# Kernel tuning notes

Hardware: AMD Instinct MI355X
Metric: run time of the kernel (lower is better)

The kernel has to match this reference:

```python
import jax, jax.numpy as jnp
import numpy as np

M = 8192        # number of variables (len(z), R is MxM)
MAX_K = 256     # max active components (self.max_k)
THRESH = 0.01   # gamma threshold used to drop topk entries


def setup_inputs() -> dict:
    key = jax.random.key(0)
    ks = jax.random.split(key, 6)
    # R is an LD-correlation-like PSD matrix (required for logdet / inverse)
    A = jax.random.normal(ks[0], (M, M), dtype=jnp.float32)
    R = A @ A.T / M + 0.1 * jnp.eye(M, dtype=jnp.float32)
    z = jax.random.normal(ks[1], (M,), dtype=jnp.float32)
    sigma2 = jax.random.uniform(ks[2], (M,), jnp.float32, 0.05, 1.0)
    p = jax.random.uniform(ks[3], (M,), jnp.float32, 0.01, 0.99)
    pq = jax.random.uniform(ks[4], (M,), jnp.float32, 0.01, 0.99)
    gamma = jax.random.uniform(ks[5], (M,), jnp.float32, 1e-4, 1.0)
    # S = inv(R) @ z, computed once in the module __init__ (a constant buffer)
    S = jnp.linalg.inv(R) @ z
    N = 100000  # GWAS sample size (python int scalar)
    return {"R": R, "z": z, "sigma2": sigma2, "p": p, "pq": pq,
            "gamma": gamma, "S": S, "N": N}


def reference(R, z, sigma2, p, pq, gamma, S, N):
    # topk + threshold filter, expressed with a fixed-size mask (jit-friendly).
    u, ind = jax.lax.top_k(gamma, MAX_K)                  # [MAX_K]
    mask = (u > THRESH).astype(R.dtype)                   # 1 for kept indices
    # U = N * diag(sigma2*gamma)[:, ind] is column-sparse: column j has single
    # nonzero vals[j] at row ind[j]. Masked columns are exactly zero, which
    # makes sigma identity in those columns, so logdet/inverse reduce to the
    # active kxk block -- identical math to the dynamic-k torch version.
    vals = N * sigma2[ind] * gamma[ind] * mask            # [MAX_K]
    Rk = R[ind]                                           # V = R[ind, :], [MAX_K, M]
    Rkk = Rk[:, ind]                                      # [MAX_K, MAX_K]
    # sigma = I_k + V @ U  (V@U collapses to Rkk scaled per-column by vals)
    sigma = jnp.eye(MAX_K, dtype=R.dtype) + Rkk * vals[None, :]
    inv = jnp.linalg.inv(sigma)
    logdet = jnp.linalg.slogdet(sigma)[1]                 # sigma is PD
    # quadratic_form = -z^T (I - U inv V) S / 2, without materializing MxM
    zU = z[ind] * vals                                    # z^T U, [MAX_K]
    VS = Rk @ S                                           # V S,   [MAX_K]
    quadratic_form = -(z @ S - zU @ (inv @ VS)) / 2
    log_likelihood = -logdet / 2 + quadratic_form
    # Bernoulli KL over the active set
    x2 = pq[ind]
    x1 = p[ind]
    kl = jnp.sum(mask * (x2 * (jnp.log(x2) - jnp.log(x1))
                         + (1 - x2) * (jnp.log(1 - x2) - jnp.log(1 - x1))))
    return -log_likelihood + kl
```

## Files before the change

kernel.cpp:

```cpp
#include <hip/hip_runtime.h>
#include <cstdint>
#include <cstddef>


#define WAVE_SYNC() asm volatile("s_waitcnt lgkmcnt(0)" ::: "memory")

__device__ __forceinline__ float bcast_lane(float v, int lane) {
  return __int_as_float(__builtin_amdgcn_readlane(__float_as_int(v), lane));
}

__global__ __launch_bounds__(256) void k_topk(
    const float* __restrict__ gamma, const float* __restrict__ sigma2,
    const float* __restrict__ z, const float* __restrict__ p,
    const float* __restrict__ pq, const int* __restrict__ Nptr,
    int* __restrict__ ind, float* __restrict__ sqv,
    float* __restrict__ t1, float* __restrict__ klt) {
  __shared__ __align__(16) float g[8 * 1032];
  int t = threadIdx.x;
  const float4* ga4 = (const float4*)gamma;
  #pragma unroll
  for (int m = 0; m < 8; ++m) {
    int i = 4 * (t + m * 256);
    float4 v = ga4[t + m * 256];
    *(float4*)&g[i + 8 * (i >> 10)] = v;
  }
  __syncthreads();
  int e = blockIdx.x * 32 + (t >> 3);
  int chunk = t & 7;
  float ge = g[e + 8 * (e >> 10)];
  const float4* g4 = (const float4*)g;
  int i4base = chunk * 258;
  int jbase = chunk * 1024;
  int cnt = 0;
  for (int it = 0; it < 256; ++it) {
    float4 v = g4[i4base + it];
    int j = jbase + 4 * it;
    cnt += (v.x > ge || (v.x == ge && (j + 0) < e)) ? 1 : 0;
    cnt += (v.y > ge || (v.y == ge && (j + 1) < e)) ? 1 : 0;
    cnt += (v.z > ge || (v.z == ge && (j + 2) < e)) ? 1 : 0;
    cnt += (v.w > ge || (v.w == ge && (j + 3) < e)) ? 1 : 0;
  }
  cnt += __shfl_xor(cnt, 1);
  cnt += __shfl_xor(cnt, 2);
  cnt += __shfl_xor(cnt, 4);
  if (chunk == 0 && cnt < 256) {
    float u = ge;
    float mask = (u > 0.01f) ? 1.0f : 0.0f;
    float fN = (float)Nptr[0];
    float vals = fN * sigma2[e] * u * mask;
    float sq = sqrtf(vals);
    ind[cnt] = e;
    sqv[cnt] = sq;
    t1[cnt] = sq * z[e];
    float x1 = p[e], x2 = pq[e];
    klt[cnt] = mask * (x2 * (logf(x2) - logf(x1)) +
                       (1.0f - x2) * (logf(1.0f - x2) - logf(1.0f - x1)));
  }
}

__global__ __launch_bounds__(256) void k_vs(
    const float* __restrict__ R, const float* __restrict__ S,
    const float* __restrict__ z, const int* __restrict__ ind,
    const float* __restrict__ sqv, float* __restrict__ M,
    float* __restrict__ t2, float* __restrict__ zS) {
  __shared__ __align__(16) float row[8192];
  __shared__ float red[4];
  int t = threadIdx.x;
  int b = blockIdx.x;
  if (b < 256) {
    int ridx = ind[b];
    const float4* Rr = (const float4*)(R + (size_t)ridx * 8192);
    const float4* S4 = (const float4*)S;
    float4* row4 = (float4*)row;
    float acc = 0.0f;
    #pragma unroll
    for (int m = 0; m < 8; ++m) {
      float4 v = Rr[t + m * 256];
      row4[t + m * 256] = v;
      float4 s = S4[t + m * 256];
      acc += v.x * s.x + v.y * s.y + v.z * s.z + v.w * s.w;
    }
    #pragma unroll
    for (int o = 32; o > 0; o >>= 1) acc += __shfl_down(acc, o);
    if ((t & 63) == 0) red[t >> 6] = acc;
    __syncthreads();
    float svb = sqv[b];
    if (t == 0) t2[b] = svb * (red[0] + red[1] + red[2] + red[3]);
    int cj = ind[t];
    float rv = row[cj];
    M[b * 256 + t] = svb * sqv[t] * rv + ((t == b) ? 1.0f : 0.0f);
  } else {
    const float4* z4 = (const float4*)z;
    const float4* S4 = (const float4*)S;
    float acc = 0.0f;
    #pragma unroll
    for (int m = 0; m < 8; ++m) {
      float4 a = z4[t + m * 256];
      float4 s = S4[t + m * 256];
      acc += a.x * s.x + a.y * s.y + a.z * s.z + a.w * s.w;
    }
    #pragma unroll
    for (int o = 32; o > 0; o >>= 1) acc += __shfl_down(acc, o);
    if ((t & 63) == 0) red[t >> 6] = acc;
    __syncthreads();
    if (t == 0) zS[0] = red[0] + red[1] + red[2] + red[3];
  }
}

__global__ __launch_bounds__(1024, 4) void k_chol(
    float* __restrict__ M, const float* __restrict__ t1w,
    const float* __restrict__ t2w, const float* __restrict__ kltw,
    const float* __restrict__ zSw, float* __restrict__ out) {
  __shared__ __align__(16) float P_cm[32 * 232];
  __shared__ __align__(16) float Ld[32 * 36];
  __shared__ float rhs1[256], rhs2[256], dv[256];
  __shared__ float idv32[32], y1[32], y2[32];
  __shared__ float red[48];
  int t = threadIdx.x;
  if (t < 256) { rhs1[t] = t1w[t]; rhs2[t] = t2w[t]; }

  for (int K = 0; K < 8; ++K) {
    int base = K * 32;
    __syncthreads();
    {
      int r = t >> 5, c = t & 31;
      Ld[r * 36 + c] = M[(size_t)(base + r) * 256 + base + c];
    }
    __syncthreads();
    if (t < 32) {
      int r = t;
      float a[32];
      #pragma unroll
      for (int c = 0; c < 32; ++c) a[c] = Ld[r * 36 + c];
      float myrt = 1.0f, myrinv = 1.0f;
      #pragma unroll
      for (int k = 0; k < 32; ++k) {
        float d = bcast_lane(a[k], k);
        float rinv = rsqrtf(d);
        float rt = d * rinv;
        float m = (r == k) ? rt : a[k] * rinv;
        if (r == k) { myrt = rt; myrinv = rinv; }
        a[k] = m;
        #pragma unroll
        for (int c = k + 1; c < 32; ++c) {
          float lck = bcast_lane(m, c);
          if (r >= c) a[c] -= m * lck;
        }
      }
      #pragma unroll
      for (int c = 0; c < 32; ++c) Ld[r * 36 + c] = a[c];
      dv[base + r] = myrt;
      idv32[r] = myrinv;
    }
    __builtin_amdgcn_wave_barrier();
    WAVE_SYNC();
    if (t < 64) {
      int r = t & 31;
      float v = (t < 32) ? rhs1[base + r] : rhs2[base + r];
      #pragma unroll
      for (int k = 0; k < 32; ++k) {
        float vk = __shfl(v, (t & 32) | k, 64);
        float yk = vk * idv32[k];
        if (r == k) v = yk;
        else if (r > k) v -= Ld[r * 36 + k] * yk;
      }
      if (t < 32) { rhs1[base + r] = v; y1[r] = v; }
      else        { rhs2[base + r] = v; y2[r] = v; }
    }
    __syncthreads();
    int nb = 224 - base;
    if (t < nb) {
      int gi = base + 32 + t;
      const float4* Mr = (const float4*)(M + (size_t)gi * 256 + base);
      float a[32];
      #pragma unroll
      for (int qq = 0; qq < 8; ++qq) {
        float4 v = Mr[qq];
        a[4*qq] = v.x; a[4*qq+1] = v.y; a[4*qq+2] = v.z; a[4*qq+3] = v.w;
      }
      float x[32];
      #pragma unroll
      for (int c = 0; c < 32; ++c) {
        float s = a[c];
        #pragma unroll
        for (int k = 0; k < c; ++k) s -= x[k] * Ld[c * 36 + k];
        x[c] = s * idv32[c];
      }
      float s1 = 0.0f, s2 = 0.0f;
      #pragma unroll
      for (int k = 0; k < 32; ++k) {
        P_cm[k * 232 + t] = x[k];
        s1 += x[k] * y1[k];
        s2 += x[k] * y2[k];
      }
      rhs1[gi] -= s1;
      rhs2[gi] -= s2;
    }
    __syncthreads();
    {
      int nbb = nb >> 3;
      int wv = t >> 6, ln = t & 63;
      int rr = ln >> 3, bcl = ln & 7;
      for (int br = wv; br < nbb; br += 16) {
        int gi = base + 32 + br * 8 + rr;
        float* Mrow = M + (size_t)gi * 256;
        for (int c0 = 0; c0 <= br; c0 += 8) {
          int bc = c0 + bcl;
          if (bc <= br) {
            int gj = base + 32 + bc * 8;
            float4 v0 = *(float4*)(Mrow + gj);
            float4 v1 = *(float4*)(Mrow + gj + 4);
            #pragma unroll
            for (int k = 0; k < 32; ++k) {
              float av = P_cm[k * 232 + br * 8 + rr];
              const float4 b0 = *(const float4*)&P_cm[k * 232 + bc * 8];
              const float4 b1 = *(const float4*)&P_cm[k * 232 + bc * 8 + 4];
              v0.x -= av * b0.x; v0.y -= av * b0.y;
              v0.z -= av * b0.z; v0.w -= av * b0.w;
              v1.x -= av * b1.x; v1.y -= av * b1.y;
              v1.z -= av * b1.z; v1.w -= av * b1.w;
            }
            *(float4*)(Mrow + gj) = v0;
            *(float4*)(Mrow + gj + 4) = v1;
          }
        }
      }
    }
  }
  __syncthreads();
  float v1 = 0.0f, v2 = 0.0f, v3 = 0.0f;
  if (t < 256) {
    v1 = logf(dv[t]);
    v2 = rhs1[t] * rhs2[t];
    v3 = kltw[t];
  }
  #pragma unroll
  for (int o = 32; o > 0; o >>= 1) {
    v1 += __shfl_down(v1, o);
    v2 += __shfl_down(v2, o);
    v3 += __shfl_down(v3, o);
  }
  if ((t & 63) == 0) {
    int w = t >> 6;
    red[w] = v1; red[16 + w] = v2; red[32 + w] = v3;
  }
  __syncthreads();
  if (t == 0) {
    float ld = 0.0f, q = 0.0f, kl = 0.0f;
    for (int w = 0; w < 16; ++w) {
      ld += red[w]; q += red[16 + w]; kl += red[32 + w];
    }
    out[0] = ld + 0.5f * (zSw[0] - q) + kl;
  }
}

extern "C" void kernel_launch(void* const* d_in, const int* in_sizes, int n_in,
                              void* d_out, int out_size, void* d_ws, size_t ws_size,
                              hipStream_t stream) {
  const float* R      = (const float*)d_in[0];
  const float* z      = (const float*)d_in[1];
  const float* sigma2 = (const float*)d_in[2];
  const float* p      = (const float*)d_in[3];
  const float* pq     = (const float*)d_in[4];
  const float* gamma  = (const float*)d_in[5];
  const float* S      = (const float*)d_in[6];
  const int*   Nptr   = (const int*)d_in[7];
  float* out = (float*)d_out;

  float* wsf = (float*)d_ws;
  float* M   = wsf;
  int*   ind = (int*)(wsf + 65536);
  float* sqv = wsf + 65536 + 256;
  float* t1  = wsf + 65536 + 512;
  float* t2  = wsf + 65536 + 768;
  float* klt = wsf + 65536 + 1024;
  float* zS  = wsf + 65536 + 1280;

  k_topk<<<256, 256, 0, stream>>>(gamma, sigma2, z, p, pq, Nptr,
                                  ind, sqv, t1, klt);
  k_vs<<<257, 256, 0, stream>>>(R, S, z, ind, sqv, M, t2, zS);
  k_chol<<<1, 1024, 0, stream>>>(M, t1, t2, klt, zS, out);
}
```

Before: 156.6 us.

## Keep packed lower-triangular matrix in LDS and use split-bf16 MFMA for trailing update

The 256x256 sigma matrix is now stored as packed lower-triangular 8x8 blocks. The Cholesky kernel copies it into LDS once, so it no longer reads and writes global memory on every panel. The trailing SYRK update now runs on 32x32 MFMA tiles, using a bf16 hi/lo split with three products to approximate fp32 accuracy in place of scalar FMA loops. The P_cm staging buffer goes away because the panel solve writes back in place. The split-bf16 scheme drops the lo*lo term, so it costs some precision, and the large LDS footprint rules out occupancy beyond one block.

After: 169.3 us. +8.1%, slower.

```diff
diff --git a/kernel.cpp b/kernel.cpp
--- a/kernel.cpp
+++ b/kernel.cpp
@@ -3,10 +3,44 @@
 #include <cstddef>
 
 
-#define WAVE_SYNC() asm volatile("s_waitcnt lgkmcnt(0)" ::: "memory")
+#define BLK_STRIDE 68
+#define PK_TOTAL (528 * BLK_STRIDE)
+
+typedef __attribute__((ext_vector_type(8))) short short8_t;
+typedef __attribute__((ext_vector_type(16))) float f32x16;
+
+__device__ __forceinline__ int blk_off(int I, int J) {
+  return (((I * (I + 1)) >> 1) + J) * BLK_STRIDE;
+}
 
 __device__ __forceinline__ float bcast_lane(float v, int lane) {
   return __int_as_float(__builtin_amdgcn_readlane(__float_as_int(v), lane));
+}
+
+__device__ __forceinline__ void split_bf16(float f, short& h, short& l) {
+  unsigned u = __float_as_uint(f);
+  unsigned hr = (u + 0x7FFFu + ((u >> 16) & 1u)) >> 16;
+  h = (short)hr;
+  float hf = __uint_as_float(hr << 16);
+  float lf = f - hf;
+  unsigned u2 = __float_as_uint(lf);
+  l = (short)((u2 + 0x7FFFu + ((u2 >> 16) & 1u)) >> 16);
+}
+
+__device__ __forceinline__ void frag_from_row(const float* Mp, int row_abs,
+                                              int kb, short8_t& hi,
+                                              short8_t& lo) {
+  int o = blk_off(row_abs >> 3, kb >> 3) + (row_abs & 7) * 8;
+  float4 v0 = *(const float4*)&Mp[o];
+  float4 v1 = *(const float4*)&Mp[o + 4];
+  float f[8] = {v0.x, v0.y, v0.z, v0.w, v1.x, v1.y, v1.z, v1.w};
+  #pragma unroll
+  for (int i = 0; i < 8; ++i) {
+    short h, l;
+    split_bf16(f[i], h, l);
+    hi[i] = h;
+    lo[i] = l;
+  }
 }
 
 __global__ __launch_bounds__(256) void k_topk(
@@ -61,7 +95,7 @@
 __global__ __launch_bounds__(256) void k_vs(
     const float* __restrict__ R, const float* __restrict__ S,
     const float* __restrict__ z, const int* __restrict__ ind,
-    const float* __restrict__ sqv, float* __restrict__ M,
+    const float* __restrict__ sqv, float* __restrict__ Mp_g,
     float* __restrict__ t2, float* __restrict__ zS) {
   __shared__ __align__(16) float row[8192];
   __shared__ float red[4];
@@ -86,9 +120,12 @@
     __syncthreads();
     float svb = sqv[b];
     if (t == 0) t2[b] = svb * (red[0] + red[1] + red[2] + red[3]);
-    int cj = ind[t];
-    float rv = row[cj];
-    M[b * 256 + t] = svb * sqv[t] * rv + ((t == b) ? 1.0f : 0.0f);
+    if ((t >> 3) <= (b >> 3)) {
+      int cj = ind[t];
+      float rv = row[cj];
+      Mp_g[blk_off(b >> 3, t >> 3) + (b & 7) * 8 + (t & 7)] =
+          svb * sqv[t] * rv + ((t == b) ? 1.0f : 0.0f);
+    }
   } else {
     const float4* z4 = (const float4*)z;
     const float4* S4 = (const float4*)S;
@@ -107,127 +144,157 @@
   }
 }
 
-__global__ __launch_bounds__(1024, 4) void k_chol(
-    float* __restrict__ M, const float* __restrict__ t1w,
+__global__ __launch_bounds__(1024) void k_chol(
+    const float* __restrict__ Mp_g, const float* __restrict__ t1w,
     const float* __restrict__ t2w, const float* __restrict__ kltw,
     const float* __restrict__ zSw, float* __restrict__ out) {
-  __shared__ __align__(16) float P_cm[32 * 232];
+  __shared__ __align__(16) float Mp[PK_TOTAL];
   __shared__ __align__(16) float Ld[32 * 36];
   __shared__ float rhs1[256], rhs2[256], dv[256];
   __shared__ float idv32[32], y1[32], y2[32];
   __shared__ float red[48];
   int t = threadIdx.x;
+
+  {
+    const float4* src = (const float4*)Mp_g;
+    float4* dst = (float4*)Mp;
+    for (int i = t; i < PK_TOTAL / 4; i += 1024) dst[i] = src[i];
+  }
   if (t < 256) { rhs1[t] = t1w[t]; rhs2[t] = t2w[t]; }
+  __syncthreads();
 
   for (int K = 0; K < 8; ++K) {
     int base = K * 32;
-    __syncthreads();
-    {
-      int r = t >> 5, c = t & 31;
-      Ld[r * 36 + c] = M[(size_t)(base + r) * 256 + base + c];
-    }
-    __syncthreads();
-    if (t < 32) {
-      int r = t;
+    int nb = 224 - base;
+    if (t < 64) {
+      if (t < 32) {
+        int r = t;
+        int I = (base >> 3) + (r >> 3);
+        float a[32];
+        #pragma unroll
+        for (int cb = 0; cb < 4; ++cb) {
+          float4 v0 = {0.f, 0.f, 0.f, 0.f}, v1 = {0.f, 0.f, 0.f, 0.f};
+          if (cb <= (r >> 3)) {
+            int o = blk_off(I, (base >> 3) + cb) + (r & 7) * 8;
+            v0 = *(const float4*)&Mp[o];
+            v1 = *(const float4*)&Mp[o + 4];
+          }
+          a[cb * 8 + 0] = v0.x; a[cb * 8 + 1] = v0.y;
+          a[cb * 8 + 2] = v0.z; a[cb * 8 + 3] = v0.w;
+          a[cb * 8 + 4] = v1.x; a[cb * 8 + 5] = v1.y;
+          a[cb * 8 + 6] = v1.z; a[cb * 8 + 7] = v1.w;
+        }
+        float myrt = 1.0f, myrinv = 1.0f;
+        #pragma unroll
+        for (int k = 0; k < 32; ++k) {
+          float d = bcast_lane(a[k], k);
+          float rinv = rsqrtf(d);
+          float rt = d * rinv;
+          float m = (r == k) ? rt : a[k] * rinv;
+          if (r == k) { myrt = rt; myrinv = rinv; }
+          a[k] = m;
+          #pragma unroll
+          for (int c = k + 1; c < 32; ++c) {
+            float lck = bcast_lane(m, c);
+            if (r >= c) a[c] -= m * lck;
+          }
+        }
+        #pragma unroll
+        for (int c = 0; c < 32; ++c) Ld[r * 36 + c] = a[c];
+        dv[base + r] = myrt;
+        idv32[r] = myrinv;
+      }
+      __builtin_amdgcn_wave_barrier();
+      asm volatile("s_waitcnt lgkmcnt(0)" ::: "memory");
+      __builtin_amdgcn_sched_barrier(0);
+      {
+        int r = t & 31;
+        float v = (t < 32) ? rhs1[base + r] : rhs2[base + r];
+        #pragma unroll
+        for (int k = 0; k < 32; ++k) {
+          float vk = __shfl(v, (t & 32) | k, 64);
+          float yk = vk * idv32[k];
+          if (r == k) v = yk;
+          else if (r > k) v -= Ld[r * 36 + k] * yk;
+        }
+        if (t < 32) { rhs1[base + r] = v; y1[r] = v; }
+        else        { rhs2[base + r] = v; y2[r] = v; }
+      }
+    }
+    __syncthreads();
+    if (nb > 0 && t < nb) {
+      int gi = base + 32 + t;
+      int I = gi >> 3, Jb = base >> 3;
       float a[32];
       #pragma unroll
-      for (int c = 0; c < 32; ++c) a[c] = Ld[r * 36 + c];
-      float myrt = 1.0f, myrinv = 1.0f;
-      #pragma unroll
-      for (int k = 0; k < 32; ++k) {
-        float d = bcast_lane(a[k], k);
-        float rinv = rsqrtf(d);
-        float rt = d * rinv;
-        float m = (r == k) ? rt : a[k] * rinv;
-        if (r == k) { myrt = rt; myrinv = rinv; }
-        a[k] = m;
-        #pragma unroll
-        for (int c = k + 1; c < 32; ++c) {
-          float lck = bcast_lane(m, c);
-          if (r >= c) a[c] -= m * lck;
-        }
-      }
-      #pragma unroll
-      for (int c = 0; c < 32; ++c) Ld[r * 36 + c] = a[c];
-      dv[base + r] = myrt;
-      idv32[r] = myrinv;
-    }
-    __builtin_amdgcn_wave_barrier();
-    WAVE_SYNC();
-    if (t < 64) {
-      int r = t & 31;
-      float v = (t < 32) ? rhs1[base + r] : rhs2[base + r];
-      #pragma unroll
-      for (int k = 0; k < 32; ++k) {
-        float vk = __shfl(v, (t & 32) | k, 64);
-        float yk = vk * idv32[k];
-        if (r == k) v = yk;
-        else if (r > k) v -= Ld[r * 36 + k] * yk;
-      }
-      if (t < 32) { rhs1[base + r] = v; y1[r] = v; }
-      else        { rhs2[base + r] = v; y2[r] = v; }
-    }
-    __syncthreads();
-    int nb = 224 - base;
-    if (t < nb) {
-      int gi = base + 32 + t;
-      const float4* Mr = (const float4*)(M + (size_t)gi * 256 + base);
-      float a[32];
-      #pragma unroll
-      for (int qq = 0; qq < 8; ++qq) {
-        float4 v = Mr[qq];
-        a[4*qq] = v.x; a[4*qq+1] = v.y; a[4*qq+2] = v.z; a[4*qq+3] = v.w;
-      }
-      float x[32];
+      for (int cb = 0; cb < 4; ++cb) {
+        int o = blk_off(I, Jb + cb) + (gi & 7) * 8;
+        float4 v0 = *(const float4*)&Mp[o];
+        float4 v1 = *(const float4*)&Mp[o + 4];
+        a[cb * 8 + 0] = v0.x; a[cb * 8 + 1] = v0.y;
+        a[cb * 8 + 2] = v0.z; a[cb * 8 + 3] = v0.w;
+        a[cb * 8 + 4] = v1.x; a[cb * 8 + 5] = v1.y;
+        a[cb * 8 + 6] = v1.z; a[cb * 8 + 7] = v1.w;
+      }
       #pragma unroll
       for (int c = 0; c < 32; ++c) {
         float s = a[c];
         #pragma unroll
-        for (int k = 0; k < c; ++k) s -= x[k] * Ld[c * 36 + k];
-        x[c] = s * idv32[c];
+        for (int k = 0; k < c; ++k) s -= a[k] * Ld[c * 36 + k];
+        a[c] = s * idv32[c];
       }
       float s1 = 0.0f, s2 = 0.0f;
       #pragma unroll
-      for (int k = 0; k < 32; ++k) {
-        P_cm[k * 232 + t] = x[k];
-        s1 += x[k] * y1[k];
-        s2 += x[k] * y2[k];
-      }
+      for (int k = 0; k < 32; ++k) { s1 += a[k] * y1[k]; s2 += a[k] * y2[k]; }
       rhs1[gi] -= s1;
       rhs2[gi] -= s2;
-    }
-    __syncthreads();
-    {
-      int nbb = nb >> 3;
-      int wv = t >> 6, ln = t & 63;
-      int rr = ln >> 3, bcl = ln & 7;
-      for (int br = wv; br < nbb; br += 16) {
-        int gi = base + 32 + br * 8 + rr;
-        float* Mrow = M + (size_t)gi * 256;
-        for (int c0 = 0; c0 <= br; c0 += 8) {
-          int bc = c0 + bcl;
-          if (bc <= br) {
-            int gj = base + 32 + bc * 8;
-            float4 v0 = *(float4*)(Mrow + gj);
-            float4 v1 = *(float4*)(Mrow + gj + 4);
-            #pragma unroll
-            for (int k = 0; k < 32; ++k) {
-              float av = P_cm[k * 232 + br * 8 + rr];
-              const float4 b0 = *(const float4*)&P_cm[k * 232 + bc * 8];
-              const float4 b1 = *(const float4*)&P_cm[k * 232 + bc * 8 + 4];
-              v0.x -= av * b0.x; v0.y -= av * b0.y;
-              v0.z -= av * b0.z; v0.w -= av * b0.w;
-              v1.x -= av * b1.x; v1.y -= av * b1.y;
-              v1.z -= av * b1.z; v1.w -= av * b1.w;
-            }
-            *(float4*)(Mrow + gj) = v0;
-            *(float4*)(Mrow + gj + 4) = v1;
+      #pragma unroll
+      for (int cb = 0; cb < 4; ++cb) {
+        int o = blk_off(I, Jb + cb) + (gi & 7) * 8;
+        float4 w0 = {a[cb * 8 + 0], a[cb * 8 + 1], a[cb * 8 + 2], a[cb * 8 + 3]};
+        float4 w1 = {a[cb * 8 + 4], a[cb * 8 + 5], a[cb * 8 + 6], a[cb * 8 + 7]};
+        *(float4*)&Mp[o] = w0;
+        *(float4*)&Mp[o + 4] = w1;
+      }
+    }
+    __syncthreads();
+    if (nb > 0) {
+      int nbb = nb >> 5;
+      int ntiles = (nbb * (nbb + 1)) >> 1;
+      int w = t >> 6, ln = t & 63;
+      int lane31 = ln & 31, kh = ln >> 5;
+      for (int idx = w; idx < ntiles; idx += 16) {
+        int ti = 0;
+        while ((((ti + 1) * (ti + 2)) >> 1) <= idx) ++ti;
+        int tj = idx - ((ti * (ti + 1)) >> 1);
+        int r_abs = base + 32 + ti * 32 + lane31;
+        int c_abs = base + 32 + tj * 32 + lane31;
+        f32x16 acc = {};
+        #pragma unroll
+        for (int k0 = 0; k0 < 2; ++k0) {
+          int kb = base + k0 * 16 + kh * 8;
+          short8_t ahi, alo, bhi, blo;
+          frag_from_row(Mp, r_abs, kb, ahi, alo);
+          frag_from_row(Mp, c_abs, kb, bhi, blo);
+          acc = __builtin_amdgcn_mfma_f32_32x32x16_bf16(ahi, bhi, acc, 0, 0, 0);
+          acc = __builtin_amdgcn_mfma_f32_32x32x16_bf16(ahi, blo, acc, 0, 0, 0);
+          acc = __builtin_amdgcn_mfma_f32_32x32x16_bf16(alo, bhi, acc, 0, 0, 0);
+        }
+        int Rb = base + 32 + ti * 32;
+        int Cc = base + 32 + tj * 32 + lane31;
+        #pragma unroll
+        for (int reg = 0; reg < 16; ++reg) {
+          int Rr = Rb + (reg & 3) + 8 * (reg >> 2) + 4 * kh;
+          if ((Cc >> 3) <= (Rr >> 3)) {
+            int o = blk_off(Rr >> 3, Cc >> 3) + (Rr & 7) * 8 + (Cc & 7);
+            Mp[o] -= acc[reg];
           }
         }
       }
     }
-  }
-  __syncthreads();
+    __syncthreads();
+  }
+
   float v1 = 0.0f, v2 = 0.0f, v3 = 0.0f;
   if (t < 256) {
     v1 = logf(dv[t]);
@@ -267,17 +334,17 @@
   const int*   Nptr   = (const int*)d_in[7];
   float* out = (float*)d_out;
 
-  float* wsf = (float*)d_ws;
-  float* M   = wsf;
-  int*   ind = (int*)(wsf + 65536);
-  float* sqv = wsf + 65536 + 256;
-  float* t1  = wsf + 65536 + 512;
-  float* t2  = wsf + 65536 + 768;
-  float* klt = wsf + 65536 + 1024;
-  float* zS  = wsf + 65536 + 1280;
+  float* wsf  = (float*)d_ws;
+  float* Mp_g = wsf;
+  int*   ind  = (int*)(wsf + PK_TOTAL);
+  float* sqv  = wsf + PK_TOTAL + 256;
+  float* t1   = wsf + PK_TOTAL + 512;
+  float* t2   = wsf + PK_TOTAL + 768;
+  float* klt  = wsf + PK_TOTAL + 1024;
+  float* zS   = wsf + PK_TOTAL + 1280;
 
   k_topk<<<256, 256, 0, stream>>>(gamma, sigma2, z, p, pq, Nptr,
                                   ind, sqv, t1, klt);
-  k_vs<<<257, 256, 0, stream>>>(R, S, z, ind, sqv, M, t2, zS);
-  k_chol<<<1, 1024, 0, stream>>>(M, t1, t2, klt, zS, out);
-}
+  k_vs<<<257, 256, 0, stream>>>(R, S, z, ind, sqv, Mp_g, t2, zS);
+  k_chol<<<1, 1024, 0, stream>>>(Mp_g, t1, t2, klt, zS, out);
+}
```
